# Performance work log

Measured on AMD Instinct MI355X. Metric: run time of the kernel, lower is better.

## Reference

```python
import jax, jax.numpy as jnp
import numpy as np

N = 50000      # nodes
E = 800000     # edges (avg degree 16)
F_IN = 128     # num_features
H = 64         # hidden_dim
G = 64         # graphs in batch


def setup_inputs() -> dict:
    key = jax.random.key(0)
    ks = jax.random.split(key, 20)
    inp = {
        "x": jax.random.normal(ks[0], (N, F_IN), jnp.float32),
        "edge_index": jax.random.randint(ks[1], (2, E), 0, N, dtype=jnp.int32).astype(jnp.int64),
        "batch": jnp.sort(jax.random.randint(ks[2], (N,), 0, G, dtype=jnp.int32)).astype(jnp.int64),
    }
    # GraphConv layer dims: in -> out
    dims = [(F_IN, H), (H, 2 * H), (2 * H, 3 * H), (3 * H, H)]
    k = 3
    for i, (din, dout) in enumerate(dims):
        s = 1.0 / np.sqrt(din).astype(np.float32)
        inp[f"w{i+1}_rel"] = jax.random.normal(ks[k], (din, dout), jnp.float32) * s
        inp[f"w{i+1}_root"] = jax.random.normal(ks[k + 1], (din, dout), jnp.float32) * s
        inp[f"b{i+1}"] = jnp.zeros((dout,), jnp.float32)
        k += 2
    inp["head_w"] = jax.random.normal(ks[k], (H, 1), jnp.float32) * (1.0 / np.sqrt(H).astype(np.float32))
    inp["head_b"] = jnp.zeros((1,), jnp.float32)
    return inp


def _graph_conv(x, src, dst, w_rel, w_root, b):
    # PyG GraphConv: out = lin_rel(sum_{j in N(i)} x_j) + lin_root(x_i)
    agg = jax.ops.segment_sum(x[src], dst, num_segments=N)  # [N, din]
    return agg @ w_rel + b + x @ w_root


def reference(x, edge_index, batch,
              w1_rel, w1_root, b1,
              w2_rel, w2_root, b2,
              w3_rel, w3_root, b3,
              w4_rel, w4_root, b4,
              head_w, head_b):
    src, dst = edge_index[0], edge_index[1]
    h = jax.nn.relu(_graph_conv(x, src, dst, w1_rel, w1_root, b1))
    h = jax.nn.relu(_graph_conv(h, src, dst, w2_rel, w2_root, b2))
    h = jax.nn.relu(_graph_conv(h, src, dst, w3_rel, w3_root, b3))
    h = _graph_conv(h, src, dst, w4_rel, w4_root, b4)          # [N, H]
    # global_mean_pool over graph ids
    sums = jax.ops.segment_sum(h, batch, num_segments=G)       # [G, H]
    counts = jax.ops.segment_sum(jnp.ones((N,), h.dtype), batch, num_segments=G)
    pooled = sums / jnp.maximum(counts, 1.0)[:, None]          # [G, H]
    return pooled @ head_w + head_b                            # [G, 1]
```

## Files before the change

### kernel.cpp

```cpp
#include <hip/hip_runtime.h>


#define NNODES 50000
#define NEDGES 800000
#define NGRAPH 64
#define NBUK 256
#define BSZ 196
#define EPB (NEDGES / NBUK)
#define CVT_NB (NNODES * 128 / 4 / 256)
#define PACK_NB (160 * 512 / 256)
#define RGRID ((NNODES + 127) / 128)
#define RCHUNK ((RGRID + 7) / 8)

typedef __attribute__((ext_vector_type(8))) __bf16 bf16x8;
typedef __attribute__((ext_vector_type(16))) float f32x16;

__device__ __forceinline__ unsigned short f2bf(float f) {
    unsigned u = __float_as_uint(f);
    u += 0x7fff + ((u >> 16) & 1);
    return (unsigned short)(u >> 16);
}
__device__ __forceinline__ float bf2f(unsigned b) {
    return __uint_as_float(b << 16);
}

__device__ __forceinline__ void dma16(const void* g, void* l) {
    __builtin_amdgcn_global_load_lds(
        (const __attribute__((address_space(1))) void*)g,
        (__attribute__((address_space(3))) void*)l, 16, 0, 0);
}


__global__ void hist_kernel(const int* __restrict__ dst, int* __restrict__ cnt) {
    __shared__ int h[NBUK];
    int tid = threadIdx.x, k = blockIdx.x;
    h[tid] = 0;
    __syncthreads();
    int end = (k + 1) * EPB;
    for (int i = k * EPB + tid; i < end; i += 256)
        atomicAdd(&h[dst[i] / BSZ], 1);
    __syncthreads();
    cnt[tid * NBUK + k] = h[tid];
}

__global__ void scan1_kernel(int* __restrict__ a, int* __restrict__ bsum, int n) {
    __shared__ int buf[256];
    int tid = threadIdx.x;
    int i = blockIdx.x * 256 + tid;
    int v = (i < n) ? a[i] : 0;
    buf[tid] = v;
    __syncthreads();
    #pragma unroll
    for (int off = 1; off < 256; off <<= 1) {
        int t = (tid >= off) ? buf[tid - off] : 0;
        __syncthreads();
        buf[tid] += t;
        __syncthreads();
    }
    if (i < n) a[i] = buf[tid] - v;
    if (tid == 255) bsum[blockIdx.x] = buf[255];
}

__global__ void scan2_kernel(int* __restrict__ bsum, int nb) {
    __shared__ int buf[256];
    int tid = threadIdx.x;
    int v = (tid < nb) ? bsum[tid] : 0;
    buf[tid] = v;
    __syncthreads();
    #pragma unroll
    for (int off = 1; off < 256; off <<= 1) {
        int t = (tid >= off) ? buf[tid - off] : 0;
        __syncthreads();
        buf[tid] += t;
        __syncthreads();
    }
    if (tid < nb) bsum[tid] = buf[tid] - v;
}

__global__ void partition_kernel(const int* __restrict__ src, const int* __restrict__ dst,
                                 const int* __restrict__ cnt, const int* __restrict__ bsum,
                                 unsigned long long* __restrict__ pedge) {
    __shared__ int lbase[NBUK];
    int tid = threadIdx.x, k = blockIdx.x;
    lbase[tid] = cnt[tid * NBUK + k] + bsum[tid];
    __syncthreads();
    int end = (k + 1) * EPB;
    for (int i = k * EPB + tid; i < end; i += 256) {
        int s = src[i], d = dst[i];
        int pos = atomicAdd(&lbase[d / BSZ], 1);
        pedge[pos] = (unsigned long long)(unsigned)s | ((unsigned long long)(unsigned)d << 32);
    }
}

__global__ void build_kernel(const unsigned long long* __restrict__ pedge,
                             const int* __restrict__ bsum,
                             int* __restrict__ rp, int* __restrict__ csr) {
    __shared__ int sdeg[256], sc[256], sbase[256], sfill[256];
    int tid = threadIdx.x, b = blockIdx.x;
    int node0 = b * BSZ;
    int ncnt = NNODES - node0;
    if (ncnt > BSZ) ncnt = BSZ;
    if (ncnt < 0) ncnt = 0;
    int seg0 = bsum[b];
    int seg1 = (b + 1 < NBUK) ? bsum[b + 1] : NEDGES;
    sdeg[tid] = 0;
    sfill[tid] = 0;
    __syncthreads();
    for (int i = seg0 + tid; i < seg1; i += 256)
        atomicAdd(&sdeg[(int)(pedge[i] >> 32) - node0], 1);
    __syncthreads();
    sc[tid] = sdeg[tid];
    __syncthreads();
    #pragma unroll
    for (int off = 1; off < 256; off <<= 1) {
        int t = (tid >= off) ? sc[tid - off] : 0;
        __syncthreads();
        sc[tid] += t;
        __syncthreads();
    }
    sbase[tid] = sc[tid] - sdeg[tid];
    if (tid < ncnt) rp[node0 + tid] = seg0 + sbase[tid];
    if (b == NBUK - 1 && tid == 0) rp[NNODES] = NEDGES;
    __syncthreads();
    for (int i = seg0 + tid; i < seg1; i += 256) {
        unsigned long long p = pedge[i];
        int d = (int)(p >> 32) - node0;
        int pos = atomicAdd(&sfill[d], 1);
        csr[seg0 + sbase[d] + pos] = (int)(p & 0xffffffffu);
    }
}


__device__ __forceinline__ void pack32(const float* __restrict__ W, unsigned short* __restrict__ dst,
                                       int KS_tot, int ks0, int dcols, int ct0,
                                       int tl, int ksl, int lane, int j) {
    int k = ksl * 16 + ((lane >> 5) << 3) + j;
    int col = tl * 32 + (lane & 31);
    dst[(((size_t)(ct0 + tl) * KS_tot + (ks0 + ksl)) * 64 + lane) * 8 + j] = f2bf(W[k * dcols + col]);
}

__global__ void prep_kernel(const float* __restrict__ x, unsigned short* __restrict__ xbf,
                            const float* __restrict__ w1_rel, const float* __restrict__ w1_root,
                            const float* __restrict__ w2_rel, const float* __restrict__ w2_root,
                            const float* __restrict__ w3_rel, const float* __restrict__ w3_root,
                            unsigned short* __restrict__ pL1, unsigned short* __restrict__ pL2,
                            unsigned short* __restrict__ pL3,
                            const float* __restrict__ w4_rel, const float* __restrict__ w4_root,
                            const float* __restrict__ b4, const float* __restrict__ head_w,
                            float* __restrict__ wr, float* __restrict__ wt,
                            float* __restrict__ cbuf) {
    int b = blockIdx.x;
    int tid = threadIdx.x;
    if (b < CVT_NB) {
        int i = b * 256 + tid;
        float4 v = ((const float4*)x)[i];
        unsigned lo = (unsigned)f2bf(v.x) | ((unsigned)f2bf(v.y) << 16);
        unsigned hi = (unsigned)f2bf(v.z) | ((unsigned)f2bf(v.w) << 16);
        ((uint2*)xbf)[i] = make_uint2(lo, hi);
    } else if (b < CVT_NB + PACK_NB) {
        int idx = (b - CVT_NB) * 256 + tid;
        int g = idx >> 9;
        int t = idx & 511;
        int lane = (t >> 3) & 63, j = t & 7;
        if (g < 16)       { int gl = g;       pack32(w1_rel,  pL1, 8,  0, 64,  0, gl / 8, gl % 8, lane, j); }
        else if (g < 32)  { int gl = g - 16;  pack32(w1_root, pL1, 8,  0, 64,  2, gl / 8, gl % 8, lane, j); }
        else if (g < 48)  { int gl = g - 32;  pack32(w2_rel,  pL2, 8,  0, 128, 0, gl / 4, gl % 4, lane, j); }
        else if (g < 64)  { int gl = g - 48;  pack32(w2_root, pL2, 8,  4, 128, 0, gl / 4, gl % 4, lane, j); }
        else if (g < 112) { int gl = g - 64;  pack32(w3_rel,  pL3, 16, 0, 192, 0, gl / 8, gl % 8, lane, j); }
        else              { int gl = g - 112; pack32(w3_root, pL3, 16, 8, 192, 0, gl / 8, gl % 8, lane, j); }
    } else {
        if (tid < 192) {
            float ar = 0.f, at = 0.f;
            for (int j = 0; j < 64; j++) {
                float hw = head_w[j];
                ar = fmaf(w4_rel[tid * 64 + j], hw, ar);
                at = fmaf(w4_root[tid * 64 + j], hw, at);
            }
            wr[tid] = ar;
            wt[tid] = at;
        } else if (tid == 192) {
            float c = 0.f;
            for (int j = 0; j < 64; j++) c = fmaf(b4[j], head_w[j], c);
            cbuf[0] = c;
        }
    }
}


template<int KS, int NT, int NHALF, int ST, int KCH>
__global__ __launch_bounds__(256) void gemm_v5(
    const unsigned short* __restrict__ A, const unsigned short* __restrict__ Wall,
    const float* __restrict__ bias, unsigned short* __restrict__ OUT,
    int ldo, int ocol0, int relu, int N,
    const float* __restrict__ wrp, const float* __restrict__ wtp,
    float* __restrict__ sb, float* __restrict__ tb)
{
    const int K = KS * 16;
    const int CPC = KCH * 2;
    __shared__ __align__(16) unsigned short sB[NT * KS * 512];
    __shared__ __align__(16) unsigned short sA[128 * KCH * 16];

    int i = blockIdx.x;
    int chunk = i / (8 * NHALF);
    int rem = i - chunk * (8 * NHALF);
    int halfsel = rem >> 3;
    int rowb = chunk * 8 + (rem & 7);
    int rbase = rowb * 128;
    if (rbase >= N) return;

    int tid = threadIdx.x;
    int wave = tid >> 6, lane = tid & 63;
    int l32 = lane & 31, half = lane >> 5;
    const unsigned short* W = Wall + (size_t)halfsel * NT * KS * 512;

    #pragma unroll
    for (int j = 0; j < NT * KS * 64 / 256; j++) {
        int p = j * 256 + wave * 64;
        dma16(W + ((size_t)p + lane) * 8, sB + (size_t)p * 8);
    }

    f32x16 acc[NT];
    #pragma unroll
    for (int t = 0; t < NT; t++)
        #pragma unroll
        for (int r = 0; r < 16; r++) acc[t][r] = 0.f;

    int lr = wave * 32 + l32;

    for (int kb = 0; kb < KS; kb += KCH) {
        if (kb > 0) __syncthreads();
        #pragma unroll
        for (int j = 0; j < 128 * CPC / 256; j++) {
            int p = j * 256 + wave * 64 + lane;
            int r = p / CPC;
            int c = p - r * CPC;
            int cg = c ^ (r & (CPC - 1));
            dma16(A + (size_t)(rbase + r) * K + kb * 16 + cg * 8,
                  sA + (size_t)(j * 256 + wave * 64) * 8);
        }
        __syncthreads();
        #pragma unroll
        for (int l = 0; l < KCH; l++) {
            int cs = (l * 2 + half) ^ (lr & (CPC - 1));
            bf16x8 a = *(const bf16x8*)(sA + (size_t)lr * (KCH * 16) + cs * 8);
            int ks = kb + l;
            #pragma unroll
            for (int t = 0; t < NT; t++) {
                bf16x8 b = *(const bf16x8*)(sB + ((size_t)(t * KS + ks) * 64 + lane) * 8);
                acc[t] = __builtin_amdgcn_mfma_f32_32x32x16_bf16(a, b, acc[t], 0, 0, 0);
            }
        }
    }

    int wrbase = rbase + wave * 32;
    if constexpr (ST) {
        #pragma unroll
        for (int reg = 0; reg < 16; reg++) {
            int row = wrbase + (reg & 3) + 8 * (reg >> 2) + 4 * half;
            float sv = 0.f, tv = 0.f;
            #pragma unroll
            for (int t = 0; t < NT; t++) {
                int col = halfsel * NT * 32 + t * 32 + l32;
                float v = fmaxf(acc[t][reg] + bias[col], 0.f);
                sv = fmaf(v, wrp[col], sv);
                tv = fmaf(v, wtp[col], tv);
            }
            #pragma unroll
            for (int m = 1; m < 32; m <<= 1) {
                sv += __shfl_xor(sv, m, 64);
                tv += __shfl_xor(tv, m, 64);
            }
            if (l32 == 0 && row < N) {
                atomicAdd(&sb[row], sv);
                atomicAdd(&tb[row], tv);
            }
        }
    } else {
        #pragma unroll
        for (int t = 0; t < NT; t++) {
            int col = t * 32 + l32;
            float bi = bias ? bias[col] : 0.f;
            #pragma unroll
            for (int reg = 0; reg < 16; reg++) {
                int row = wrbase + (reg & 3) + 8 * (reg >> 2) + 4 * half;
                if (row < N) {
                    float v = acc[t][reg] + bi;
                    if (relu) v = fmaxf(v, 0.f);
                    OUT[(size_t)row * ldo + ocol0 + col] = f2bf(v);
                }
            }
        }
    }
}


__device__ __forceinline__ void acc8(float* a, uint4 u) {
    a[0] += bf2f(u.x & 0xffffu); a[1] += bf2f(u.x >> 16);
    a[2] += bf2f(u.y & 0xffffu); a[3] += bf2f(u.y >> 16);
    a[4] += bf2f(u.z & 0xffffu); a[5] += bf2f(u.z >> 16);
    a[6] += bf2f(u.w & 0xffffu); a[7] += bf2f(u.w >> 16);
}

template<int LPF, int SUBS>
__global__ void agg_kernel_v4(const unsigned short* __restrict__ X, int ldx,
                              const int* __restrict__ rp, const int* __restrict__ csr,
                              const unsigned short* __restrict__ root, int ldr,
                              const float* __restrict__ bias, int relu,
                              unsigned short* __restrict__ OUT, int ldo, int N) {
    int t = blockIdx.x * blockDim.x + threadIdx.x;
    int node = t / (SUBS * LPF);
    int r = t % (SUBS * LPF);
    int sub = r / LPF;
    int sl = r % LPF;
    if (node >= N) return;
    float a[8] = {0.f, 0.f, 0.f, 0.f, 0.f, 0.f, 0.f, 0.f};
    int e0 = rp[node], e1 = rp[node + 1];
    const unsigned short* xb = X + 8 * sl;
    int e = e0 + sub;
    for (; e + 3 * SUBS < e1; e += 4 * SUBS) {
        int s0 = csr[e], s1 = csr[e + SUBS], s2 = csr[e + 2 * SUBS], s3 = csr[e + 3 * SUBS];
        uint4 u0 = *(const uint4*)(xb + (size_t)s0 * ldx);
        uint4 u1 = *(const uint4*)(xb + (size_t)s1 * ldx);
        uint4 u2 = *(const uint4*)(xb + (size_t)s2 * ldx);
        uint4 u3 = *(const uint4*)(xb + (size_t)s3 * ldx);
        acc8(a, u0); acc8(a, u1); acc8(a, u2); acc8(a, u3);
    }
    for (; e < e1; e += SUBS) {
        uint4 u = *(const uint4*)(xb + (size_t)csr[e] * ldx);
        acc8(a, u);
    }
    #pragma unroll
    for (int m = LPF; m < SUBS * LPF; m <<= 1)
        #pragma unroll
        for (int i = 0; i < 8; i++) a[i] += __shfl_xor(a[i], m, 64);
    if (sub == 0) {
        if (root) {
            uint4 u = *(const uint4*)(root + (size_t)node * ldr + 8 * sl);
            acc8(a, u);
        }
        if (bias) {
            float4 b0 = *(const float4*)(bias + 8 * sl);
            float4 b1 = *(const float4*)(bias + 8 * sl + 4);
            a[0] += b0.x; a[1] += b0.y; a[2] += b0.z; a[3] += b0.w;
            a[4] += b1.x; a[5] += b1.y; a[6] += b1.z; a[7] += b1.w;
        }
        if (relu) {
            #pragma unroll
            for (int i = 0; i < 8; i++) a[i] = fmaxf(a[i], 0.f);
        }
        uint4 o;
        o.x = (unsigned)f2bf(a[0]) | ((unsigned)f2bf(a[1]) << 16);
        o.y = (unsigned)f2bf(a[2]) | ((unsigned)f2bf(a[3]) << 16);
        o.z = (unsigned)f2bf(a[4]) | ((unsigned)f2bf(a[5]) << 16);
        o.w = (unsigned)f2bf(a[6]) | ((unsigned)f2bf(a[7]) << 16);
        *(uint4*)(OUT + (size_t)node * ldo + 8 * sl) = o;
    }
}


__global__ void aggpool_kernel(const float* __restrict__ s, const float* __restrict__ t,
                               const int* __restrict__ rp, const int* __restrict__ csr,
                               const int* __restrict__ batch, float* __restrict__ gsum,
                               int* __restrict__ cnt, int N) {
    __shared__ float ls[NGRAPH];
    __shared__ int lc[NGRAPH];
    int tid = threadIdx.x;
    if (tid < NGRAPH) { ls[tid] = 0.f; lc[tid] = 0; }
    __syncthreads();
    int n = blockIdx.x * blockDim.x + tid;
    if (n < N) {
        float a = 0.f;
        int e = rp[n], e1 = rp[n + 1];
        for (; e + 3 < e1; e += 4) {
            int s0 = csr[e], s1 = csr[e + 1], s2 = csr[e + 2], s3 = csr[e + 3];
            a += s[s0] + s[s1] + s[s2] + s[s3];
        }
        for (; e < e1; e++) a += s[csr[e]];
        int g = batch[n];
        atomicAdd(&ls[g], a + t[n]);
        atomicAdd(&lc[g], 1);
    }
    __syncthreads();
    if (tid < NGRAPH && lc[tid] > 0) {
        atomicAdd(&gsum[tid], ls[tid]);
        atomicAdd(&cnt[tid], lc[tid]);
    }
}

__global__ void final_kernel(const float* __restrict__ gsum, const int* __restrict__ cnt,
                             const float* __restrict__ cbuf, const float* __restrict__ head_b,
                             float* __restrict__ out) {
    int g = threadIdx.x;
    if (g < NGRAPH) {
        float c = (float)(cnt[g] > 0 ? cnt[g] : 1);
        out[g] = gsum[g] / c + cbuf[0] + head_b[0];
    }
}


extern "C" void kernel_launch(void* const* d_in, const int* in_sizes, int n_in,
                              void* d_out, int out_size, void* d_ws, size_t ws_size,
                              hipStream_t stream) {
    const float* x       = (const float*)d_in[0];
    const int*   edge    = (const int*)d_in[1];
    const int*   batch   = (const int*)d_in[2];
    const float* w1_rel  = (const float*)d_in[3];
    const float* w1_root = (const float*)d_in[4];
    const float* b1      = (const float*)d_in[5];
    const float* w2_rel  = (const float*)d_in[6];
    const float* w2_root = (const float*)d_in[7];
    const float* b2      = (const float*)d_in[8];
    const float* w3_rel  = (const float*)d_in[9];
    const float* w3_root = (const float*)d_in[10];
    const float* b3      = (const float*)d_in[11];
    const float* w4_rel  = (const float*)d_in[12];
    const float* w4_root = (const float*)d_in[13];
    const float* b4      = (const float*)d_in[14];
    const float* head_w  = (const float*)d_in[15];
    const float* head_b  = (const float*)d_in[16];
    float* out = (float*)d_out;

    const int N = NNODES, E = NEDGES;
    const int* esrc = edge;
    const int* edst = edge + E;

    char* ws = (char*)d_ws;
    size_t off = 0;
    auto alloc = [&](size_t bytes) -> char* {
        char* p = ws + off;
        off = (off + bytes + 255) & ~(size_t)255;
        return p;
    };
    float* gsum  = (float*)alloc(NGRAPH * 4);
    int*   cnt   = (int*)alloc(NGRAPH * 4);
    float* sbuf  = (float*)alloc((size_t)N * 4);
    float* tbuf  = (float*)alloc((size_t)N * 4);
    size_t zero_bytes = off;
    int*   bcnt  = (int*)alloc((size_t)NBUK * NBUK * 4);
    int*   bsum  = (int*)alloc(256 * 4);
    int*   rp    = (int*)alloc((size_t)(N + 1) * 4);
    int*   csr   = (int*)alloc((size_t)E * 4);
    unsigned long long* pedge = (unsigned long long*)alloc((size_t)E * 8);
    unsigned short* xbf    = (unsigned short*)alloc((size_t)N * 128 * 2);
    unsigned short* z1     = (unsigned short*)alloc((size_t)N * 128 * 2);
    unsigned short* combo2 = (unsigned short*)alloc((size_t)N * 128 * 2);
    unsigned short* combo3 = (unsigned short*)alloc((size_t)N * 256 * 2);
    unsigned short* pL1    = (unsigned short*)alloc(4 * 8 * 512 * 2);
    unsigned short* pL2    = (unsigned short*)alloc(4 * 8 * 512 * 2);
    unsigned short* pL3    = (unsigned short*)alloc(6 * 16 * 512 * 2);
    float* wr    = (float*)alloc(192 * 4);
    float* wt    = (float*)alloc(192 * 4);
    float* cbuf  = (float*)alloc(4);
    (void)ws_size;

    hipMemsetAsync(gsum, 0, zero_bytes, stream);

    const int TB = 256;

    hist_kernel<<<NBUK, 256, 0, stream>>>(edst, bcnt);
    scan1_kernel<<<NBUK, 256, 0, stream>>>(bcnt, bsum, NBUK * NBUK);
    scan2_kernel<<<1, 256, 0, stream>>>(bsum, NBUK);
    partition_kernel<<<NBUK, 256, 0, stream>>>(esrc, edst, bcnt, bsum, pedge);
    build_kernel<<<NBUK, 256, 0, stream>>>(pedge, bsum, rp, csr);

    prep_kernel<<<CVT_NB + PACK_NB + 1, 256, 0, stream>>>(
        x, xbf, w1_rel, w1_root, w2_rel, w2_root, w3_rel, w3_root,
        pL1, pL2, pL3, w4_rel, w4_root, b4, head_w, wr, wt, cbuf);

    gemm_v5<8, 4, 1, 0, 8><<<RCHUNK * 8, 256, 0, stream>>>(
        xbf, pL1, nullptr, z1, 128, 0, 0, N, nullptr, nullptr, nullptr, nullptr);
    agg_kernel_v4<8, 2><<<(N * 16 + TB - 1) / TB, TB, 0, stream>>>(z1, 128, rp, csr,
                                                                   z1 + 64, 128, b1, 1, combo2 + 64, 128, N);
    agg_kernel_v4<8, 2><<<(N * 16 + TB - 1) / TB, TB, 0, stream>>>(combo2 + 64, 128, rp, csr,
                                                                   nullptr, 0, nullptr, 0, combo2, 128, N);
    gemm_v5<8, 4, 1, 0, 8><<<RCHUNK * 8, 256, 0, stream>>>(
        combo2, pL2, b2, combo3, 256, 128, 1, N, nullptr, nullptr, nullptr, nullptr);
    agg_kernel_v4<16, 2><<<(N * 32 + TB - 1) / TB, TB, 0, stream>>>(combo3 + 128, 256, rp, csr,
                                                                    nullptr, 0, nullptr, 0, combo3, 256, N);
    gemm_v5<16, 3, 2, 1, 4><<<RCHUNK * 8 * 2, 256, 0, stream>>>(
        combo3, pL3, b3, nullptr, 0, 0, 0, N, wr, wt, sbuf, tbuf);

    aggpool_kernel<<<(N + TB - 1) / TB, TB, 0, stream>>>(sbuf, tbuf, rp, csr, batch, gsum, cnt, N);
    final_kernel<<<1, 64, 0, stream>>>(gsum, cnt, cbuf, head_b, out);
}
```

Measured before the change: 251.9 us.

## Fuse histogram, bucket scan and prep into one kernel with last-block scan

Merges the edge-bucket histogram, both scan kernels and the feature/weight prep kernel into a single launch, where the last block to finish (tracked by an atomic counter) scans the global bucket counts. The partition kernel now recounts its local buckets and claims output ranges with global atomics instead of reading a per-block prefix table. This removes four launches and the 256x256 count matrix, at the cost of rereading dst in partition and making the edge order within buckets nondeterministic.

```diff
diff --git a/kernel.cpp b/kernel.cpp
--- a/kernel.cpp
+++ b/kernel.cpp
@@ -9,6 +9,7 @@
 #define EPB (NEDGES / NBUK)
 #define CVT_NB (NNODES * 128 / 4 / 256)
 #define PACK_NB (160 * 512 / 256)
+#define PREP_NB (CVT_NB + PACK_NB + 1)
 #define RGRID ((NNODES + 127) / 128)
 #define RCHUNK ((RGRID + 7) / 8)
 
@@ -28,106 +29,6 @@
     __builtin_amdgcn_global_load_lds(
         (const __attribute__((address_space(1))) void*)g,
         (__attribute__((address_space(3))) void*)l, 16, 0, 0);
-}
-
-
-__global__ void hist_kernel(const int* __restrict__ dst, int* __restrict__ cnt) {
-    __shared__ int h[NBUK];
-    int tid = threadIdx.x, k = blockIdx.x;
-    h[tid] = 0;
-    __syncthreads();
-    int end = (k + 1) * EPB;
-    for (int i = k * EPB + tid; i < end; i += 256)
-        atomicAdd(&h[dst[i] / BSZ], 1);
-    __syncthreads();
-    cnt[tid * NBUK + k] = h[tid];
-}
-
-__global__ void scan1_kernel(int* __restrict__ a, int* __restrict__ bsum, int n) {
-    __shared__ int buf[256];
-    int tid = threadIdx.x;
-    int i = blockIdx.x * 256 + tid;
-    int v = (i < n) ? a[i] : 0;
-    buf[tid] = v;
-    __syncthreads();
-    #pragma unroll
-    for (int off = 1; off < 256; off <<= 1) {
-        int t = (tid >= off) ? buf[tid - off] : 0;
-        __syncthreads();
-        buf[tid] += t;
-        __syncthreads();
-    }
-    if (i < n) a[i] = buf[tid] - v;
-    if (tid == 255) bsum[blockIdx.x] = buf[255];
-}
-
-__global__ void scan2_kernel(int* __restrict__ bsum, int nb) {
-    __shared__ int buf[256];
-    int tid = threadIdx.x;
-    int v = (tid < nb) ? bsum[tid] : 0;
-    buf[tid] = v;
-    __syncthreads();
-    #pragma unroll
-    for (int off = 1; off < 256; off <<= 1) {
-        int t = (tid >= off) ? buf[tid - off] : 0;
-        __syncthreads();
-        buf[tid] += t;
-        __syncthreads();
-    }
-    if (tid < nb) bsum[tid] = buf[tid] - v;
-}
-
-__global__ void partition_kernel(const int* __restrict__ src, const int* __restrict__ dst,
-                                 const int* __restrict__ cnt, const int* __restrict__ bsum,
-                                 unsigned long long* __restrict__ pedge) {
-    __shared__ int lbase[NBUK];
-    int tid = threadIdx.x, k = blockIdx.x;
-    lbase[tid] = cnt[tid * NBUK + k] + bsum[tid];
-    __syncthreads();
-    int end = (k + 1) * EPB;
-    for (int i = k * EPB + tid; i < end; i += 256) {
-        int s = src[i], d = dst[i];
-        int pos = atomicAdd(&lbase[d / BSZ], 1);
-        pedge[pos] = (unsigned long long)(unsigned)s | ((unsigned long long)(unsigned)d << 32);
-    }
-}
-
-__global__ void build_kernel(const unsigned long long* __restrict__ pedge,
-                             const int* __restrict__ bsum,
-                             int* __restrict__ rp, int* __restrict__ csr) {
-    __shared__ int sdeg[256], sc[256], sbase[256], sfill[256];
-    int tid = threadIdx.x, b = blockIdx.x;
-    int node0 = b * BSZ;
-    int ncnt = NNODES - node0;
-    if (ncnt > BSZ) ncnt = BSZ;
-    if (ncnt < 0) ncnt = 0;
-    int seg0 = bsum[b];
-    int seg1 = (b + 1 < NBUK) ? bsum[b + 1] : NEDGES;
-    sdeg[tid] = 0;
-    sfill[tid] = 0;
-    __syncthreads();
-    for (int i = seg0 + tid; i < seg1; i += 256)
-        atomicAdd(&sdeg[(int)(pedge[i] >> 32) - node0], 1);
-    __syncthreads();
-    sc[tid] = sdeg[tid];
-    __syncthreads();
-    #pragma unroll
-    for (int off = 1; off < 256; off <<= 1) {
-        int t = (tid >= off) ? sc[tid - off] : 0;
-        __syncthreads();
-        sc[tid] += t;
-        __syncthreads();
-    }
-    sbase[tid] = sc[tid] - sdeg[tid];
-    if (tid < ncnt) rp[node0 + tid] = seg0 + sbase[tid];
-    if (b == NBUK - 1 && tid == 0) rp[NNODES] = NEDGES;
-    __syncthreads();
-    for (int i = seg0 + tid; i < seg1; i += 256) {
-        unsigned long long p = pedge[i];
-        int d = (int)(p >> 32) - node0;
-        int pos = atomicAdd(&sfill[d], 1);
-        csr[seg0 + sbase[d] + pos] = (int)(p & 0xffffffffu);
-    }
 }
 
 
@@ -139,18 +40,15 @@
     dst[(((size_t)(ct0 + tl) * KS_tot + (ks0 + ksl)) * 64 + lane) * 8 + j] = f2bf(W[k * dcols + col]);
 }
 
-__global__ void prep_kernel(const float* __restrict__ x, unsigned short* __restrict__ xbf,
-                            const float* __restrict__ w1_rel, const float* __restrict__ w1_root,
-                            const float* __restrict__ w2_rel, const float* __restrict__ w2_root,
-                            const float* __restrict__ w3_rel, const float* __restrict__ w3_root,
-                            unsigned short* __restrict__ pL1, unsigned short* __restrict__ pL2,
-                            unsigned short* __restrict__ pL3,
-                            const float* __restrict__ w4_rel, const float* __restrict__ w4_root,
-                            const float* __restrict__ b4, const float* __restrict__ head_w,
-                            float* __restrict__ wr, float* __restrict__ wt,
-                            float* __restrict__ cbuf) {
-    int b = blockIdx.x;
-    int tid = threadIdx.x;
+__device__ void prep_body(int b, int tid,
+                          const float* x, unsigned short* xbf,
+                          const float* w1_rel, const float* w1_root,
+                          const float* w2_rel, const float* w2_root,
+                          const float* w3_rel, const float* w3_root,
+                          unsigned short* pL1, unsigned short* pL2, unsigned short* pL3,
+                          const float* w4_rel, const float* w4_root,
+                          const float* b4, const float* head_w,
+                          float* wr, float* wt, float* cbuf) {
     if (b < CVT_NB) {
         int i = b * 256 + tid;
         float4 v = ((const float4*)x)[i];
@@ -187,6 +85,120 @@
 }
 
 
+__global__ void __launch_bounds__(256) histprep_kernel(
+    const int* __restrict__ edst, int* __restrict__ gcount,
+    int* __restrict__ bsum, int* __restrict__ roff, int* __restrict__ done,
+    const float* __restrict__ x, unsigned short* __restrict__ xbf,
+    const float* __restrict__ w1_rel, const float* __restrict__ w1_root,
+    const float* __restrict__ w2_rel, const float* __restrict__ w2_root,
+    const float* __restrict__ w3_rel, const float* __restrict__ w3_root,
+    unsigned short* __restrict__ pL1, unsigned short* __restrict__ pL2,
+    unsigned short* __restrict__ pL3,
+    const float* __restrict__ w4_rel, const float* __restrict__ w4_root,
+    const float* __restrict__ b4, const float* __restrict__ head_w,
+    float* __restrict__ wr, float* __restrict__ wt, float* __restrict__ cbuf)
+{
+    __shared__ int sm[256];
+    __shared__ int lastflag;
+    int tid = threadIdx.x, b = blockIdx.x;
+    if (b < NBUK) {
+        sm[tid] = 0;
+        __syncthreads();
+        int end = (b + 1) * EPB;
+        for (int i = b * EPB + tid; i < end; i += 256)
+            atomicAdd(&sm[edst[i] / BSZ], 1);
+        __syncthreads();
+        if (sm[tid]) atomicAdd(&gcount[tid], sm[tid]);
+    } else {
+        prep_body(b - NBUK, tid, x, xbf, w1_rel, w1_root, w2_rel, w2_root,
+                  w3_rel, w3_root, pL1, pL2, pL3, w4_rel, w4_root, b4, head_w,
+                  wr, wt, cbuf);
+    }
+    __threadfence();
+    __syncthreads();
+    if (tid == 0) {
+        int d = atomicAdd(done, 1);
+        lastflag = (d == (int)gridDim.x - 1);
+    }
+    __syncthreads();
+    if (lastflag) {
+        int v = atomicAdd(&gcount[tid], 0);
+        sm[tid] = v;
+        __syncthreads();
+        #pragma unroll
+        for (int off = 1; off < 256; off <<= 1) {
+            int t = (tid >= off) ? sm[tid - off] : 0;
+            __syncthreads();
+            sm[tid] += t;
+            __syncthreads();
+        }
+        int base = sm[tid] - v;
+        bsum[tid] = base;
+        roff[tid] = base;
+    }
+}
+
+
+__global__ void partition_kernel(const int* __restrict__ esrc, const int* __restrict__ edst,
+                                 int* __restrict__ roff,
+                                 unsigned long long* __restrict__ pedge) {
+    __shared__ int cur[NBUK];
+    int tid = threadIdx.x, k = blockIdx.x;
+    cur[tid] = 0;
+    __syncthreads();
+    int end = (k + 1) * EPB;
+    for (int i = k * EPB + tid; i < end; i += 256)
+        atomicAdd(&cur[edst[i] / BSZ], 1);
+    __syncthreads();
+    int cnt = cur[tid];
+    cur[tid] = cnt ? atomicAdd(&roff[tid], cnt) : 0;
+    __syncthreads();
+    for (int i = k * EPB + tid; i < end; i += 256) {
+        int s = esrc[i], d = edst[i];
+        int pos = atomicAdd(&cur[d / BSZ], 1);
+        pedge[pos] = (unsigned long long)(unsigned)s | ((unsigned long long)(unsigned)d << 32);
+    }
+}
+
+__global__ void build_kernel(const unsigned long long* __restrict__ pedge,
+                             const int* __restrict__ bsum,
+                             int* __restrict__ rp, int* __restrict__ csr) {
+    __shared__ int sdeg[256], sc[256], sbase[256], sfill[256];
+    int tid = threadIdx.x, b = blockIdx.x;
+    int node0 = b * BSZ;
+    int ncnt = NNODES - node0;
+    if (ncnt > BSZ) ncnt = BSZ;
+    if (ncnt < 0) ncnt = 0;
+    int seg0 = bsum[b];
+    int seg1 = (b + 1 < NBUK) ? bsum[b + 1] : NEDGES;
+    sdeg[tid] = 0;
+    sfill[tid] = 0;
+    __syncthreads();
+    for (int i = seg0 + tid; i < seg1; i += 256)
+        atomicAdd(&sdeg[(int)(pedge[i] >> 32) - node0], 1);
+    __syncthreads();
+    sc[tid] = sdeg[tid];
+    __syncthreads();
+    #pragma unroll
+    for (int off = 1; off < 256; off <<= 1) {
+        int t = (tid >= off) ? sc[tid - off] : 0;
+        __syncthreads();
+        sc[tid] += t;
+        __syncthreads();
+    }
+    sbase[tid] = sc[tid] - sdeg[tid];
+    if (tid < ncnt) rp[node0 + tid] = seg0 + sbase[tid];
+    if (b == NBUK - 1 && tid == 0) rp[NNODES] = NEDGES;
+    __syncthreads();
+    for (int i = seg0 + tid; i < seg1; i += 256) {
+        unsigned long long p = pedge[i];
+        int d = (int)(p >> 32) - node0;
+        int pos = atomicAdd(&sfill[d], 1);
+        csr[seg0 + sbase[d] + pos] = (int)(p & 0xffffffffu);
+    }
+}
+
+
 template<int KS, int NT, int NHALF, int ST, int KCH>
 __global__ __launch_bounds__(256) void gemm_v5(
     const unsigned short* __restrict__ A, const unsigned short* __restrict__ Wall,
@@ -431,13 +443,15 @@
         off = (off + bytes + 255) & ~(size_t)255;
         return p;
     };
-    float* gsum  = (float*)alloc(NGRAPH * 4);
-    int*   cnt   = (int*)alloc(NGRAPH * 4);
-    float* sbuf  = (float*)alloc((size_t)N * 4);
-    float* tbuf  = (float*)alloc((size_t)N * 4);
+    float* gsum   = (float*)alloc(NGRAPH * 4);
+    int*   cnt    = (int*)alloc(NGRAPH * 4);
+    float* sbuf   = (float*)alloc((size_t)N * 4);
+    float* tbuf   = (float*)alloc((size_t)N * 4);
+    int*   gcount = (int*)alloc(NBUK * 4);
+    int*   done   = (int*)alloc(4);
     size_t zero_bytes = off;
-    int*   bcnt  = (int*)alloc((size_t)NBUK * NBUK * 4);
-    int*   bsum  = (int*)alloc(256 * 4);
+    int*   bsum  = (int*)alloc(NBUK * 4);
+    int*   roff  = (int*)alloc(NBUK * 4);
     int*   rp    = (int*)alloc((size_t)(N + 1) * 4);
     int*   csr   = (int*)alloc((size_t)E * 4);
     unsigned long long* pedge = (unsigned long long*)alloc((size_t)E * 8);
@@ -457,15 +471,12 @@
 
     const int TB = 256;
 
-    hist_kernel<<<NBUK, 256, 0, stream>>>(edst, bcnt);
-    scan1_kernel<<<NBUK, 256, 0, stream>>>(bcnt, bsum, NBUK * NBUK);
-    scan2_kernel<<<1, 256, 0, stream>>>(bsum, NBUK);
-    partition_kernel<<<NBUK, 256, 0, stream>>>(esrc, edst, bcnt, bsum, pedge);
+    histprep_kernel<<<NBUK + PREP_NB, 256, 0, stream>>>(
+        edst, gcount, bsum, roff, done, x, xbf,
+        w1_rel, w1_root, w2_rel, w2_root, w3_rel, w3_root,
+        pL1, pL2, pL3, w4_rel, w4_root, b4, head_w, wr, wt, cbuf);
+    partition_kernel<<<NBUK, 256, 0, stream>>>(esrc, edst, roff, pedge);
     build_kernel<<<NBUK, 256, 0, stream>>>(pedge, bsum, rp, csr);
-
-    prep_kernel<<<CVT_NB + PACK_NB + 1, 256, 0, stream>>>(
-        x, xbf, w1_rel, w1_root, w2_rel, w2_root, w3_rel, w3_root,
-        pL1, pL2, pL3, w4_rel, w4_root, b4, head_w, wr, wt, cbuf);
 
     gemm_v5<8, 4, 1, 0, 8><<<RCHUNK * 8, 256, 0, stream>>>(
         xbf, pL1, nullptr, z1, 128, 0, 0, N, nullptr, nullptr, nullptr, nullptr);
```

New measurement: 732.4 us. 2.91x slower.
